# Kernel tuning notes

Measured on AMD Instinct MI355X. Metric: run time of the kernel, lower is better.

## Reference

```python
import jax, jax.numpy as jnp
from jax import lax
import numpy as np

B, N = 8, 8192
NPOINT, RADIUS, NSAMPLE = 2048, 0.4, 64
EPS = 1e-5


def setup_inputs() -> dict:
    key = jax.random.key(0)
    ks = jax.random.split(key, 8)
    d = {
        'xyz': jax.random.normal(ks[0], (B, N, 3), jnp.float32),
        'features': jax.random.normal(ks[1], (B, 64, N), jnp.float32),
        'W0': jax.random.normal(ks[2], (64, 67), jnp.float32) * 0.1,
        'g0': jnp.ones((64,), jnp.float32), 'b0': jnp.zeros((64,), jnp.float32),
        'm0': jnp.zeros((64,), jnp.float32), 'v0': jnp.ones((64,), jnp.float32),
        'W1': jax.random.normal(ks[3], (64, 64), jnp.float32) * 0.1,
        'g1': jnp.ones((64,), jnp.float32), 'b1': jnp.zeros((64,), jnp.float32),
        'm1': jnp.zeros((64,), jnp.float32), 'v1': jnp.ones((64,), jnp.float32),
        'W2': jax.random.normal(ks[4], (128, 64), jnp.float32) * 0.1,
        'g2': jnp.ones((128,), jnp.float32), 'b2': jnp.zeros((128,), jnp.float32),
        'm2': jnp.zeros((128,), jnp.float32), 'v2': jnp.ones((128,), jnp.float32),
    }
    return d


def fps(xyz, npoint):
    # sequential furthest point sampling, start at index 0 (as in CUDA op)
    b = xyz.shape[0]
    first = jnp.zeros((b,), jnp.int32)
    d0 = jnp.sum((xyz - xyz[:, :1]) ** 2, -1)  # (B,N) dist to point 0

    def body(dist, _):
        nxt = jnp.argmax(dist, -1).astype(jnp.int32)
        p = jnp.take_along_axis(xyz, nxt[:, None, None].astype(jnp.int32), axis=1)
        dist = jnp.minimum(dist, jnp.sum((xyz - p) ** 2, -1))
        return dist, nxt

    _, rest = lax.scan(body, d0, None, length=npoint - 1)  # rest: (npoint-1, B)
    return jnp.concatenate([first[:, None], rest.T], axis=1)  # (B, npoint)


def ball_query(xyz, new_xyz, radius, nsample):
    # (B,P,N) squared distances
    d2 = jnp.sum((new_xyz[:, :, None, :] - xyz[:, None, :, :]) ** 2, -1)
    mask = d2 < radius * radius
    # stable sort: in-radius indices first, in original order (matches CUDA fill order)
    order = jnp.argsort(jnp.where(mask, 0, 1).astype(jnp.int32), axis=-1, stable=True)
    idx = order[..., :nsample]
    cnt = jnp.sum(mask, -1)  # (B,P)
    pos = jnp.arange(nsample)
    return jnp.where(pos < cnt[..., None], idx, idx[..., :1])  # pad with first found


def group(x, idx):
    # x (B,N,D), idx (B,P,S) -> (B,P,S,D)
    return jnp.take_along_axis(x[:, None], idx[..., None], axis=2)


def reference(xyz, features, W0, g0, b0, m0, v0, W1, g1, b1, m1, v1, W2, g2, b2, m2, v2):
    inds = fps(xyz, NPOINT)                                   # (B,P)
    new_xyz = jnp.take_along_axis(xyz, inds[..., None], axis=1)  # (B,P,3)
    idx = ball_query(xyz, new_xyz, RADIUS, NSAMPLE)           # (B,P,S)
    gxyz = group(xyz, idx) - new_xyz[:, :, None, :]           # (B,P,S,3) centered
    gfeat = group(jnp.swapaxes(features, 1, 2), idx)          # (B,P,S,C)
    x = jnp.concatenate([gxyz, gfeat], -1)                    # use_xyz concat
    x = jnp.transpose(x, (0, 3, 1, 2))                        # (B,C+3,P,S)
    for W, g, b, m, v in ((W0, g0, b0, m0, v0), (W1, g1, b1, m1, v1), (W2, g2, b2, m2, v2)):
        x = jnp.einsum('oi,bips->bops', W, x)                 # 1x1 conv
        scale = g / jnp.sqrt(v + EPS)
        x = (x - m[:, None, None]) * scale[:, None, None] + b[:, None, None]
        x = jax.nn.relu(x)
    new_features = jnp.max(x, -1)                             # max pool over nsample -> (B,128,P)
    return new_xyz, new_features, inds
```

## Files before the change

kernel.cpp:

```cpp
#include <hip/hip_runtime.h>
#include <cstdint>
#include <cstddef>

#define BATCH   8
#define NPTS    8192
#define NPOINT  2048
#define NSAMPLE 64
#define K0      67
#define C2      128

typedef float v2f __attribute__((ext_vector_type(2)));

__device__ __forceinline__ float d2e(float ax, float ay, float az,
                                     float bx, float by, float bz) {
#pragma clang fp contract(off)
  float dx = ax - bx;
  float dy = ay - by;
  float dz = az - bz;
  float t0 = dx * dx;
  float t1 = dy * dy;
  float t2 = dz * dz;
  return (t0 + t1) + t2;
}

__device__ __forceinline__ unsigned long long dpp_min_key(unsigned long long k) {
#define KSTEP(CTRL, RM, BM)                                                    \
  {                                                                            \
    int lo = (int)k, hi = (int)(k >> 32);                                      \
    int lo2 = __builtin_amdgcn_update_dpp(lo, lo, CTRL, RM, BM, false);        \
    int hi2 = __builtin_amdgcn_update_dpp(hi, hi, CTRL, RM, BM, false);        \
    unsigned long long k2 =                                                    \
        ((unsigned long long)(unsigned)hi2 << 32) | (unsigned)lo2;             \
    k = (k2 < k) ? k2 : k;                                                     \
  }
  KSTEP(0xB1, 0xF, 0xF)
  KSTEP(0x4E, 0xF, 0xF)
  KSTEP(0x141, 0xF, 0xF)
  KSTEP(0x140, 0xF, 0xF)
  KSTEP(0x142, 0xA, 0xF)
  KSTEP(0x143, 0xC, 0xF)
#undef KSTEP
  int lo = __builtin_amdgcn_readlane((int)k, 63);
  int hi = __builtin_amdgcn_readlane((int)(k >> 32), 63);
  return ((unsigned long long)(unsigned)hi << 32) | (unsigned)lo;
}

__global__ __launch_bounds__(512) void fps_kernel(const float* __restrict__ xyz,
                                                  float* __restrict__ out_xyz,
                                                  float* __restrict__ out_inds) {
  const int b = blockIdx.x;
  const int tid = threadIdx.x;
  const int lane = tid & 63, w = tid >> 6;

  __shared__ float2 sxy[NPTS];
  __shared__ float  szl[NPTS];
  __shared__ unsigned short sslot[NPOINT];
  __shared__ unsigned long long wred[2][8] __attribute__((aligned(16)));

  const float* xb = xyz + (size_t)b * NPTS * 3;

  for (int k = 0; k < 16; k++) {
    int i = tid + k * 512;
    sxy[i] = make_float2(xb[i * 3 + 0], xb[i * 3 + 1]);
    szl[i] = xb[i * 3 + 2];
  }
  __syncthreads();

  const float2 q0xy = sxy[0];
  const float q0x = q0xy.x, q0y = q0xy.y, q0z = szl[0];

  const int base = tid * 16;
  v2f px2[8], py2[8], pz2[8], dd2[8];
  {
#pragma clang fp contract(off)
#pragma unroll
    for (int k = 0; k < 8; k++) {
      float2 a = sxy[base + 2 * k];
      float2 c = sxy[base + 2 * k + 1];
      px2[k] = (v2f){a.x, c.x};
      py2[k] = (v2f){a.y, c.y};
      pz2[k] = (v2f){szl[base + 2 * k], szl[base + 2 * k + 1]};
      v2f dx = px2[k] - q0x;
      v2f dy = py2[k] - q0y;
      v2f dz = pz2[k] - q0z;
      v2f t0 = dx * dx;
      v2f t1 = dy * dy;
      v2f t2 = dz * dz;
      dd2[k] = (t0 + t1) + t2;
    }
  }
  if (tid == 0) sslot[0] = 0;

  {
    float bv = -1.f; int bj = base;
#pragma unroll
    for (int k = 0; k < 8; k++) {
      float d0 = dd2[k].x, d1 = dd2[k].y;
      bool c0 = d0 > bv; bv = c0 ? d0 : bv; bj = c0 ? base + 2 * k : bj;
      bool c1 = d1 > bv; bv = c1 ? d1 : bv; bj = c1 ? base + 2 * k + 1 : bj;
    }
    unsigned long long kk =
        ((unsigned long long)(~__float_as_uint(bv)) << 13) | (unsigned)bj;
    kk = dpp_min_key(kk);
    if (lane == 0) wred[0][w] = kk;
  }
  __syncthreads();

  for (int t = 1; t < NPOINT; ++t) {
    const ulonglong2* wv = (const ulonglong2*)wred[(t - 1) & 1];
    ulonglong2 p0 = wv[0], p1 = wv[1], p2 = wv[2], p3 = wv[3];
    unsigned long long g0 = (p0.y < p0.x) ? p0.y : p0.x;
    unsigned long long g1 = (p1.y < p1.x) ? p1.y : p1.x;
    unsigned long long g2 = (p2.y < p2.x) ? p2.y : p2.x;
    unsigned long long g3 = (p3.y < p3.x) ? p3.y : p3.x;
    g0 = (g1 < g0) ? g1 : g0; g2 = (g3 < g2) ? g3 : g2;
    g0 = (g2 < g0) ? g2 : g0;
    const int nxt = (int)(g0 & 0x1FFFu);
    const float2 qxy = sxy[nxt];
    const float qx = qxy.x, qy = qxy.y, qz = szl[nxt];
    if (tid == 0) sslot[t] = (unsigned short)nxt;

    float bv = -1.f; int bj = base;
    {
#pragma clang fp contract(off)
#pragma unroll
      for (int k = 0; k < 8; k++) {
        v2f dx = px2[k] - qx;
        v2f dy = py2[k] - qy;
        v2f dz = pz2[k] - qz;
        v2f t0 = dx * dx;
        v2f t1 = dy * dy;
        v2f t2 = dz * dz;
        v2f d = (t0 + t1) + t2;
        v2f nd;
        nd.x = fminf(dd2[k].x, d.x);
        nd.y = fminf(dd2[k].y, d.y);
        dd2[k] = nd;
        bool c0 = nd.x > bv; bv = c0 ? nd.x : bv; bj = c0 ? base + 2 * k : bj;
        bool c1 = nd.y > bv; bv = c1 ? nd.y : bv; bj = c1 ? base + 2 * k + 1 : bj;
      }
    }
    unsigned long long kk =
        ((unsigned long long)(~__float_as_uint(bv)) << 13) | (unsigned)bj;
    kk = dpp_min_key(kk);
    if (lane == 0) wred[t & 1][w] = kk;
    __syncthreads();
  }

  for (int t = tid; t < NPOINT; t += 512) {
    int o = (int)sslot[t];
    float2 xy = sxy[o];
    out_inds[b * NPOINT + t] = (float)o;
    out_xyz[((size_t)b * NPOINT + t) * 3 + 0] = xy.x;
    out_xyz[((size_t)b * NPOINT + t) * 3 + 1] = xy.y;
    out_xyz[((size_t)b * NPOINT + t) * 3 + 2] = szl[o];
  }
}

__global__ __launch_bounds__(128) void prep_kernel(
    const float* __restrict__ W0, const float* __restrict__ g0,
    const float* __restrict__ b0, const float* __restrict__ m0,
    const float* __restrict__ v0, const float* __restrict__ g1,
    const float* __restrict__ b1, const float* __restrict__ m1,
    const float* __restrict__ v1, const float* __restrict__ g2,
    const float* __restrict__ b2, const float* __restrict__ m2,
    const float* __restrict__ v2, float* __restrict__ wsp) {
  const int tid = threadIdx.x;
  if (tid < 64) {
    float s0 = g0[tid] / sqrtf(v0[tid] + 1e-5f);
    wsp[4 * tid + 0] = s0 * W0[tid * K0 + 0];
    wsp[4 * tid + 1] = s0 * W0[tid * K0 + 1];
    wsp[4 * tid + 2] = s0 * W0[tid * K0 + 2];
    wsp[4 * tid + 3] = b0[tid] - m0[tid] * s0;
    wsp[640 + tid] = s0;
    float s1 = g1[tid] / sqrtf(v1[tid] + 1e-5f);
    wsp[256 + tid] = s1; wsp[320 + tid] = b1[tid] - m1[tid] * s1;
  }
  float s2 = g2[tid] / sqrtf(v2[tid] + 1e-5f);
  wsp[384 + tid] = s2; wsp[512 + tid] = b2[tid] - m2[tid] * s2;
}

__global__ __launch_bounds__(256) void zfeat_kernel(const float* __restrict__ xyz,
                                                    const float* __restrict__ feat,
                                                    const float* __restrict__ W0,
                                                    const float* __restrict__ wsp,
                                                    float* __restrict__ szp) {
  __shared__ float ftile[64][64];
  __shared__ float sxyz[192];
  const int bt = blockIdx.x;
  const int b = bt >> 7, nt = bt & 127;
  const int tid = threadIdx.x;
  const int lane = tid & 63, w = tid >> 6;

  const float* fb = feat + (size_t)b * 64 * NPTS + (size_t)nt * 64;
#pragma unroll
  for (int r = w; r < 64; r += 4)
    ftile[r][lane] = fb[(size_t)r * NPTS + lane];
  if (tid < 192)
    sxyz[tid] = xyz[((size_t)b * NPTS + (size_t)nt * 64) * 3 + tid];

  float w0x = W0[lane * K0 + 0], w0y = W0[lane * K0 + 1], w0z = W0[lane * K0 + 2];
  float wf[64];
#pragma unroll
  for (int i = 0; i < 64; i++) wf[i] = W0[lane * K0 + 3 + i];
  const float s0 = wsp[640 + lane];
  __syncthreads();

  float* ob = szp + ((size_t)b * NPTS + (size_t)nt * 64) * 64;
  for (int u = w; u < 64; u += 4) {
    float acc = w0x * sxyz[u * 3 + 0] + w0y * sxyz[u * 3 + 1] + w0z * sxyz[u * 3 + 2];
#pragma unroll
    for (int i = 0; i < 64; i++) acc = fmaf(wf[i], ftile[i][u], acc);
    ob[(size_t)u * 64 + lane] = acc * s0;
  }
}

#define QPW 4
__global__ __launch_bounds__(256, 2) void mlp_kernel(
    const float* __restrict__ xyz, const float* __restrict__ szp,
    const float* __restrict__ new_xyz, const float* __restrict__ W1,
    const float* __restrict__ W2, const float* __restrict__ wsp,
    float* __restrict__ out_feat) {
  __shared__ float ylds[4][64];
  __shared__ int   blds[4][64];
  const int tid = threadIdx.x;
  const int lane = tid & 63, wid = tid >> 6;

  float4 w1v[16], w2av[16], w2bv[16];
  const float4* W1r = (const float4*)(W1 + lane * 64);
  const float4* W2ar = (const float4*)(W2 + lane * 64);
  const float4* W2br = (const float4*)(W2 + (lane + 64) * 64);
#pragma unroll
  for (int i = 0; i < 16; i++) { w1v[i] = W1r[i]; w2av[i] = W2ar[i]; w2bv[i] = W2br[i]; }
  const float4 A = ((const float4*)wsp)[lane];
  const float sc1l = wsp[256 + lane], sh1l = wsp[320 + lane];
  const float sc2al = wsp[384 + lane], sh2al = wsp[512 + lane];
  const float sc2bl = wsp[448 + lane], sh2bl = wsp[576 + lane];
  const float RR = (float)(0.4 * 0.4);

  int* bl = blds[wid];
  const float4* yv = (const float4*)ylds[wid];

  for (int qi = 0; qi < QPW; qi++) {
    const int q = blockIdx.x * (4 * QPW) + qi * 4 + wid;
    const int b = q >> 11, p = q & 2047;
    const float* xb = xyz + (size_t)b * NPTS * 3;
    const float* szb = szp + (size_t)b * NPTS * 64;

    const float cx = new_xyz[(size_t)q * 3 + 0];
    const float cy = new_xyz[(size_t)q * 3 + 1];
    const float cz = new_xyz[(size_t)q * 3 + 2];
    const float hc = A.w - (A.x * cx + A.y * cy + A.z * cz);

    int cnt = 0, firsti = -1;
    for (int base2 = 0; base2 < NPTS; base2 += 64) {
      int i = base2 + lane;
      float xx = xb[i * 3 + 0], yy = xb[i * 3 + 1], zz = xb[i * 3 + 2];
      float dq = d2e(xx, yy, zz, cx, cy, cz);
      bool m = dq < RR;
      unsigned long long mask = __ballot(m);
      if (mask) {
        if (firsti < 0) firsti = base2 + (__ffsll((unsigned long long)mask) - 1);
        int pos = cnt + (int)__popcll(mask & ((1ull << lane) - 1ull));
        if (m && pos < NSAMPLE) bl[pos] = i;
        cnt += (int)__popcll(mask);
        if (cnt >= NSAMPLE) break;
      }
    }
    for (int s = cnt + lane; s < NSAMPLE; s += 64) bl[s] = firsti;
    __builtin_amdgcn_s_waitcnt(0);

    float vA = 0.f, vB = 0.f;
    int idx0 = bl[0];
    float fcur = szb[(size_t)idx0 * 64 + lane];

    for (int s = 0; s < NSAMPLE; s++) {
      int sn = (s < NSAMPLE - 1) ? s + 1 : s;
      int idxn = bl[sn];
      float fnext = szb[(size_t)idxn * 64 + lane];

      float y0 = fmaxf(fcur + hc, 0.f);
      ylds[wid][lane] = y0;
      float a0 = 0.f, a1 = 0.f, a2 = 0.f, a3 = 0.f;
#pragma unroll
      for (int i = 0; i < 16; i++) {
        float4 y = yv[i];
        a0 = fmaf(w1v[i].x, y.x, a0);
        a1 = fmaf(w1v[i].y, y.y, a1);
        a2 = fmaf(w1v[i].z, y.z, a2);
        a3 = fmaf(w1v[i].w, y.w, a3);
      }
      float y1 = fmaxf(fmaf((a0 + a1) + (a2 + a3), sc1l, sh1l), 0.f);
      ylds[wid][lane] = y1;
      float c0 = 0.f, c1 = 0.f, c2 = 0.f, c3 = 0.f;
      float e0 = 0.f, e1 = 0.f, e2 = 0.f, e3 = 0.f;
#pragma unroll
      for (int i = 0; i < 16; i++) {
        float4 y = yv[i];
        c0 = fmaf(w2av[i].x, y.x, c0);
        c1 = fmaf(w2av[i].y, y.y, c1);
        c2 = fmaf(w2av[i].z, y.z, c2);
        c3 = fmaf(w2av[i].w, y.w, c3);
        e0 = fmaf(w2bv[i].x, y.x, e0);
        e1 = fmaf(w2bv[i].y, y.y, e1);
        e2 = fmaf(w2bv[i].z, y.z, e2);
        e3 = fmaf(w2bv[i].w, y.w, e3);
      }
      float y2a = fmaxf(fmaf((c0 + c1) + (c2 + c3), sc2al, sh2al), 0.f);
      float y2b = fmaxf(fmaf((e0 + e1) + (e2 + e3), sc2bl, sh2bl), 0.f);
      vA = fmaxf(vA, y2a);
      vB = fmaxf(vB, y2b);
      fcur = fnext;
    }
    out_feat[((size_t)b * C2 + lane) * NPOINT + p] = vA;
    out_feat[((size_t)b * C2 + lane + 64) * NPOINT + p] = vB;
  }
}

extern "C" void kernel_launch(void* const* d_in, const int* in_sizes, int n_in,
                              void* d_out, int out_size, void* d_ws, size_t ws_size,
                              hipStream_t stream) {
  const float* xyz  = (const float*)d_in[0];
  const float* feat = (const float*)d_in[1];
  const float* W0 = (const float*)d_in[2];
  const float* g0 = (const float*)d_in[3];
  const float* b0 = (const float*)d_in[4];
  const float* m0 = (const float*)d_in[5];
  const float* v0 = (const float*)d_in[6];
  const float* W1 = (const float*)d_in[7];
  const float* g1 = (const float*)d_in[8];
  const float* b1 = (const float*)d_in[9];
  const float* m1 = (const float*)d_in[10];
  const float* v1 = (const float*)d_in[11];
  const float* W2 = (const float*)d_in[12];
  const float* g2 = (const float*)d_in[13];
  const float* b2 = (const float*)d_in[14];
  const float* m2 = (const float*)d_in[15];
  const float* v2 = (const float*)d_in[16];

  float* out = (float*)d_out;
  float* out_xyz  = out;
  float* out_feat = out + 49152;
  float* out_inds = out + 49152 + 2097152;

  float* szp  = (float*)((char*)d_ws + 4194304);
  float* wsp  = (float*)((char*)d_ws + 20971520);

  hipLaunchKernelGGL(prep_kernel, dim3(1), dim3(128), 0, stream,
                     W0, g0, b0, m0, v0, g1, b1, m1, v1, g2, b2, m2, v2, wsp);
  hipLaunchKernelGGL(zfeat_kernel, dim3(BATCH * (NPTS / 64)), dim3(256), 0, stream,
                     xyz, feat, W0, wsp, szp);
  hipLaunchKernelGGL(fps_kernel, dim3(BATCH), dim3(512), 0, stream,
                     xyz, out_xyz, out_inds);
  hipLaunchKernelGGL(mlp_kernel, dim3((BATCH * NPOINT) / (4 * QPW)), dim3(256), 0, stream,
                     xyz, szp, out_xyz, W1, W2, wsp, out_feat);
}
```

Before: 2.646 ms.

## Split ball query out of MLP kernel into separate kernel

Moves the radius ball query from the register-heavy MLP kernel into its own lightweight kernel. That kernel writes neighbor indices to a workspace buffer, and the MLP kernel then loads them. The ball search gets its own launch with higher occupancy for the latency-bound scan over xyz, so it no longer runs at the MLP kernel's low occupancy. The cost is an extra kernel launch plus a global round trip for the index buffer.

```diff
diff --git a/kernel.cpp b/kernel.cpp
--- a/kernel.cpp
+++ b/kernel.cpp
@@ -215,9 +215,39 @@
   }
 }
 
+__global__ __launch_bounds__(256) void ballq_kernel(const float* __restrict__ xyz,
+                                                    const float* __restrict__ new_xyz,
+                                                    int* __restrict__ ball) {
+  const int lane = threadIdx.x & 63;
+  const int q = blockIdx.x * 4 + (threadIdx.x >> 6);
+  const int b = q >> 11;
+  const float RR = (float)(0.4 * 0.4);
+  const float cx = new_xyz[(size_t)q * 3 + 0];
+  const float cy = new_xyz[(size_t)q * 3 + 1];
+  const float cz = new_xyz[(size_t)q * 3 + 2];
+  const float* xb = xyz + (size_t)b * NPTS * 3;
+  int cnt = 0, firsti = -1;
+  for (int base = 0; base < NPTS; base += 64) {
+    int i = base + lane;
+    float xx = xb[i * 3 + 0], yy = xb[i * 3 + 1], zz = xb[i * 3 + 2];
+    float d2 = d2e(xx, yy, zz, cx, cy, cz);
+    bool m = d2 < RR;
+    unsigned long long mask = __ballot(m);
+    if (mask) {
+      if (firsti < 0) firsti = base + (__ffsll((unsigned long long)mask) - 1);
+      int pos = cnt + (int)__popcll(mask & ((1ull << lane) - 1ull));
+      if (m && pos < NSAMPLE) ball[(size_t)q * NSAMPLE + pos] = i;
+      cnt += (int)__popcll(mask);
+      if (cnt >= NSAMPLE) break;
+    }
+  }
+  for (int s = cnt + lane; s < NSAMPLE; s += 64)
+    ball[(size_t)q * NSAMPLE + s] = firsti;
+}
+
 #define QPW 4
 __global__ __launch_bounds__(256, 2) void mlp_kernel(
-    const float* __restrict__ xyz, const float* __restrict__ szp,
+    const float* __restrict__ szp, const int* __restrict__ ball,
     const float* __restrict__ new_xyz, const float* __restrict__ W1,
     const float* __restrict__ W2, const float* __restrict__ wsp,
     float* __restrict__ out_feat) {
@@ -236,47 +266,28 @@
   const float sc1l = wsp[256 + lane], sh1l = wsp[320 + lane];
   const float sc2al = wsp[384 + lane], sh2al = wsp[512 + lane];
   const float sc2bl = wsp[448 + lane], sh2bl = wsp[576 + lane];
-  const float RR = (float)(0.4 * 0.4);
-
-  int* bl = blds[wid];
-  const float4* yv = (const float4*)ylds[wid];
 
   for (int qi = 0; qi < QPW; qi++) {
     const int q = blockIdx.x * (4 * QPW) + qi * 4 + wid;
     const int b = q >> 11, p = q & 2047;
-    const float* xb = xyz + (size_t)b * NPTS * 3;
-    const float* szb = szp + (size_t)b * NPTS * 64;
 
     const float cx = new_xyz[(size_t)q * 3 + 0];
     const float cy = new_xyz[(size_t)q * 3 + 1];
     const float cz = new_xyz[(size_t)q * 3 + 2];
     const float hc = A.w - (A.x * cx + A.y * cy + A.z * cz);
 
-    int cnt = 0, firsti = -1;
-    for (int base2 = 0; base2 < NPTS; base2 += 64) {
-      int i = base2 + lane;
-      float xx = xb[i * 3 + 0], yy = xb[i * 3 + 1], zz = xb[i * 3 + 2];
-      float dq = d2e(xx, yy, zz, cx, cy, cz);
-      bool m = dq < RR;
-      unsigned long long mask = __ballot(m);
-      if (mask) {
-        if (firsti < 0) firsti = base2 + (__ffsll((unsigned long long)mask) - 1);
-        int pos = cnt + (int)__popcll(mask & ((1ull << lane) - 1ull));
-        if (m && pos < NSAMPLE) bl[pos] = i;
-        cnt += (int)__popcll(mask);
-        if (cnt >= NSAMPLE) break;
-      }
-    }
-    for (int s = cnt + lane; s < NSAMPLE; s += 64) bl[s] = firsti;
+    blds[wid][lane] = ball[(size_t)q * NSAMPLE + lane];
+    const float* szb = szp + (size_t)b * NPTS * 64;
     __builtin_amdgcn_s_waitcnt(0);
 
     float vA = 0.f, vB = 0.f;
-    int idx0 = bl[0];
+    int idx0 = blds[wid][0];
     float fcur = szb[(size_t)idx0 * 64 + lane];
+    const float4* yv = (const float4*)ylds[wid];
 
     for (int s = 0; s < NSAMPLE; s++) {
       int sn = (s < NSAMPLE - 1) ? s + 1 : s;
-      int idxn = bl[sn];
+      int idxn = blds[wid][sn];
       float fnext = szb[(size_t)idxn * 64 + lane];
 
       float y0 = fmaxf(fcur + hc, 0.f);
@@ -343,6 +354,7 @@
   float* out_feat = out + 49152;
   float* out_inds = out + 49152 + 2097152;
 
+  int*   ball = (int*)d_ws;
   float* szp  = (float*)((char*)d_ws + 4194304);
   float* wsp  = (float*)((char*)d_ws + 20971520);
 
@@ -352,6 +364,8 @@
                      xyz, feat, W0, wsp, szp);
   hipLaunchKernelGGL(fps_kernel, dim3(BATCH), dim3(512), 0, stream,
                      xyz, out_xyz, out_inds);
+  hipLaunchKernelGGL(ballq_kernel, dim3((BATCH * NPOINT) / 4), dim3(256), 0, stream,
+                     xyz, out_xyz, ball);
   hipLaunchKernelGGL(mlp_kernel, dim3((BATCH * NPOINT) / (4 * QPW)), dim3(256), 0, stream,
-                     xyz, szp, out_xyz, W1, W2, wsp, out_feat);
-}
+                     szp, ball, out_xyz, W1, W2, wsp, out_feat);
+}
```

After: 2.520 ms. -4.8%, faster.
